# Optimization experiments

Measured on AMD Instinct MI355X. Metric: run time of the kernel, lower is better.

Reference implementation:

```python
import jax, jax.numpy as jnp
import numpy as np

TREE_DEPTH = 6
TEMPERATURE = 1.0


def setup_inputs() -> dict:
    key = jax.random.key(0)
    k1, k2, k3, k4, k5 = jax.random.split(key, 5)
    B, D = 8192, 512
    T = 64                      # n_trees
    N = 2 ** TREE_DEPTH - 1    # internal nodes = 63
    L = 2 ** TREE_DEPTH        # leaves = 64
    C = 100                    # classes
    return {
        "x": jax.random.normal(k1, (B, D), dtype=jnp.float32),
        "split_weights": jax.random.normal(k2, (T, N, D), dtype=jnp.float32),
        "split_bias": jax.random.normal(k3, (T, N), dtype=jnp.float32),
        "leaf_logits": jax.random.normal(k4, (T, L, C), dtype=jnp.float32),
        "tree_weights": jax.random.uniform(k5, (T,), dtype=jnp.float32),
    }


def reference(x, split_weights, split_bias, leaf_logits, tree_weights):
    # All node decisions for all trees in one batched GEMM: [B, T, N]
    dec = jax.nn.sigmoid(
        (jnp.einsum("bd,tnd->btn", x, split_weights) + split_bias) / TEMPERATURE
    )
    B = x.shape[0]
    T = split_weights.shape[0]
    L = leaf_logits.shape[1]  # 2 ** TREE_DEPTH
    leaf_ids = jnp.arange(L)
    # Cumulative product of routing probs along each leaf's root-to-leaf path.
    leaf_probs = jnp.ones((B, T, L), dtype=x.dtype)
    for d in range(TREE_DEPTH):
        # ancestor node (level order) of each leaf at this depth
        node_idx = (2 ** d - 1) + (leaf_ids >> (TREE_DEPTH - d))
        # 1 -> right child (prob = dec), 0 -> left child (prob = 1 - dec)
        bit = (leaf_ids >> (TREE_DEPTH - d - 1)) & 1
        dd = dec[:, :, node_idx]  # [B, T, L]
        leaf_probs = leaf_probs * jnp.where(bit.astype(bool), dd, 1.0 - dd)
    tree_out = jax.nn.softmax(leaf_logits, axis=-1)  # [T, L, C]
    # weighted sum over trees of (leaf_probs @ leaf class dists)
    return jnp.einsum("btl,tlc,t->bc", leaf_probs, tree_out, tree_weights)
```

## Files before the change

### kernel.cpp

```cpp
#include <hip/hip_runtime.h>

#define TREES 64
#define NN 63
#define LL 64
#define CC 100
#define CPAD 112
#define DD 512
#define BB 8192

typedef __attribute__((ext_vector_type(8))) _Float16 f16x8;
typedef __attribute__((ext_vector_type(4))) _Float16 f16x4;
typedef __attribute__((ext_vector_type(4))) float floatx4;

#define XH_WS   0
#define SWH_WS  8388608
#define W2T_WS  12582912

__device__ __forceinline__ void gl_lds16(const _Float16* g, char* lds) {
    __builtin_amdgcn_global_load_lds(
        (const __attribute__((address_space(1))) unsigned int*)g,
        (__attribute__((address_space(3))) unsigned int*)lds, 16, 0, 0);
}

__device__ __forceinline__ f16x8 cvt8(const float* s) {
    float4 a = *(const float4*)s, b = *(const float4*)(s + 4);
    f16x8 h;
    h[0]=(_Float16)a.x; h[1]=(_Float16)a.y; h[2]=(_Float16)a.z; h[3]=(_Float16)a.w;
    h[4]=(_Float16)b.x; h[5]=(_Float16)b.y; h[6]=(_Float16)b.z; h[7]=(_Float16)b.w;
    return h;
}

__device__ __forceinline__ float fsig(float x) {
    return __builtin_amdgcn_rcpf(1.f + __expf(-x));
}

__global__ __launch_bounds__(256) void prep_kernel(
    const float* __restrict__ x, const float* __restrict__ sw,
    const float* __restrict__ leaf_logits, const float* __restrict__ tree_w,
    _Float16* __restrict__ xh, _Float16* __restrict__ swh,
    _Float16* __restrict__ w2T, float* __restrict__ out)
{
    if (blockIdx.x < 3072) {
        int i = blockIdx.x * 256 + threadIdx.x;
        if (i < 524288) {
            int tile = i >> 10, cidx = i & 1023;
            int row = cidx >> 3, c = cidx & 7;
            int rb = tile >> 3, kt = tile & 7;
            int gk = kt * 64 + ((c ^ (row & 7)) << 3);
            *(f16x8*)(xh + (size_t)i * 8) = cvt8(x + (size_t)(rb * 128 + row) * DD + gk);
        } else {
            int j = i - 524288;
            if (j < 262144) {
                int tile = j >> 10, cidx = j & 1023;
                int col = cidx >> 3, c = cidx & 7;
                int cb = tile >> 3, kt = tile & 7;
                int tt = col >> 6, node = col & 63;
                f16x8 h = (f16x8)(_Float16)0.f;
                if (node < NN) {
                    int gk = kt * 64 + ((c ^ (col & 7)) << 3);
                    h = cvt8(sw + (size_t)((cb * 2 + tt) * NN + node) * DD + gk);
                }
                *(f16x8*)(swh + (size_t)j * 8) = h;
            }
        }
    } else if (blockIdx.x < 4096) {
        int row  = (blockIdx.x - 3072) * 4 + (threadIdx.x >> 6);
        int lane = threadIdx.x & 63;
        int t = row >> 6, l = row & 63;
        const float* src = leaf_logits + (size_t)row * CC;
        float v0 = (lane < CC)      ? src[lane]      : -1e30f;
        float v1 = (lane + 64 < CC) ? src[lane + 64] : -1e30f;
        float m = fmaxf(v0, v1);
#pragma unroll
        for (int off = 32; off > 0; off >>= 1)
            m = fmaxf(m, __shfl_down(m, off, 64));
        m = __shfl(m, 0, 64);
        float e0 = (lane < CC)      ? __expf(v0 - m) : 0.f;
        float e1 = (lane + 64 < CC) ? __expf(v1 - m) : 0.f;
        float s = e0 + e1;
#pragma unroll
        for (int off = 32; off > 0; off >>= 1)
            s += __shfl_down(s, off, 64);
        s = __shfl(s, 0, 64);
        float scale = tree_w[t] / s;
        _Float16* base = w2T + (size_t)t * CPAD * LL;
#define LSWZ(c) ((((l >> 3) ^ ((c) & 7)) << 3) | (l & 7))
        if (lane < CC)      base[(size_t)lane * LL + LSWZ(lane)]               = (_Float16)(e0 * scale);
        if (lane + 64 < CC) base[(size_t)(lane + 64) * LL + LSWZ(lane + 64)]   = (_Float16)(e1 * scale);
        if (lane < CPAD - CC) base[(size_t)(CC + lane) * LL + LSWZ(CC + lane)] = (_Float16)0.f;
#undef LSWZ
    } else {
        int i = (blockIdx.x - 4096) * 1024 + threadIdx.x * 4;
        *(float4*)(out + i) = make_float4(0.f, 0.f, 0.f, 0.f);
    }
}

#define A_SMEM 33280
__global__ __launch_bounds__(256, 2) void fused_kernel(
    const _Float16* __restrict__ xh,
    const _Float16* __restrict__ swh,
    const float* __restrict__ sb,
    const _Float16* __restrict__ w2T,
    float* __restrict__ out)
{
    __shared__ __align__(16) char smem[A_SMEM];
    _Float16* xs  = (_Float16*)smem;
    _Float16* wl  = (_Float16*)(smem + 16384);
    _Float16* dec = (_Float16*)smem;
    _Float16* lpl = (_Float16*)smem;

    const int tid  = threadIdx.x;
    const int lane = tid & 63;
    const int wid  = tid >> 6;
    const int wy   = wid >> 1;
    const int wx   = wid & 1;
    const int quad = lane >> 4;
    const int l15  = lane & 15;
    const int rb   = blockIdx.x;
    const int tc   = blockIdx.y;

    floatx4 oacc2[2][7];
#pragma unroll
    for (int mi = 0; mi < 2; ++mi)
#pragma unroll
        for (int ni = 0; ni < 7; ++ni) oacc2[mi][ni] = (floatx4)0.f;

    const _Float16* xtile = xh + (size_t)rb * 8 * 8192;

    for (int tg = 0; tg < 4; ++tg) {
        const int cb = tc * 4 + tg;
        const _Float16* wtile = swh + (size_t)cb * 8 * 8192;

        float bias_v[4];
        {
            int mytree = cb * 2 + wx;
#pragma unroll
            for (int ni = 0; ni < 4; ++ni) {
                int nd = 16 * ni + l15;
                bias_v[ni] = (nd < NN) ? sb[mytree * NN + nd] : 0.f;
            }
        }

        floatx4 acc[4][4];
#pragma unroll
        for (int i = 0; i < 4; ++i)
#pragma unroll
            for (int j = 0; j < 4; ++j) acc[i][j] = (floatx4)0.f;

        for (int kt = 0; kt < 8; ++kt) {
            __syncthreads();
#pragma unroll
            for (int j = 0; j < 4; ++j) {
                gl_lds16(xtile + kt * 8192 + j * 2048 + wid * 512 + lane * 8,
                         smem + j * 4096 + wid * 1024);
                gl_lds16(wtile + kt * 8192 + j * 2048 + wid * 512 + lane * 8,
                         smem + 16384 + j * 4096 + wid * 1024);
            }
            __syncthreads();
#pragma unroll
            for (int ks = 0; ks < 2; ++ks) {
                f16x8 af[4], bf[4];
#pragma unroll
                for (int mi = 0; mi < 4; ++mi) {
                    int r = 64 * wy + 16 * mi + l15;
                    af[mi] = *(const f16x8*)&xs[r * 64 + ((((ks << 2) | quad) ^ (r & 7)) << 3)];
                }
#pragma unroll
                for (int ni = 0; ni < 4; ++ni) {
                    int r = 64 * wx + 16 * ni + l15;
                    bf[ni] = *(const f16x8*)&wl[r * 64 + ((((ks << 2) | quad) ^ (r & 7)) << 3)];
                }
#pragma unroll
                for (int mi = 0; mi < 4; ++mi)
#pragma unroll
                    for (int ni = 0; ni < 4; ++ni)
                        acc[mi][ni] = __builtin_amdgcn_mfma_f32_16x16x32_f16(
                            af[mi], bf[ni], acc[mi][ni], 0, 0, 0);
            }
        }
        __syncthreads();

#pragma unroll
        for (int mi = 0; mi < 4; ++mi) {
            int r0 = 64 * wy + 16 * mi + 4 * quad;
#pragma unroll
            for (int ni = 0; ni < 4; ++ni) {
                int col = 64 * wx + 16 * ni + l15;
                f16x4 v;
#pragma unroll
                for (int r = 0; r < 4; ++r)
                    v[r] = (_Float16)(acc[mi][ni][r] + bias_v[ni]);
                *(f16x4*)&dec[col * 130 + r0] = v;
            }
        }
        __syncthreads();

        const int tt   = tid >> 7;
        const int lrow = tid & 127;
        const int tb   = tt * 64;
        f16x8 lpreg[8];
        {
#define SIG(n) fsig((float)dec[(tb + (n)) * 130 + lrow])
            float d0 = SIG(0);
#pragma unroll
            for (int h = 0; h < 2; ++h) {
                float p1 = h ? d0 : 1.f - d0;
                float d1 = SIG(1 + h);
#pragma unroll
                for (int b8 = 0; b8 < 4; ++b8) {
                    int i4 = b8 >> 1, i3 = b8 & 1;
                    float p2 = p1 * (i4 ? d1 : 1.f - d1);
                    float d2 = SIG(3 + 2 * h + i4);
                    float p3 = p2 * (i3 ? d2 : 1.f - d2);
                    float d3 = SIG(7 + 4 * h + b8);
                    f16x8 blk;
#pragma unroll
                    for (int i2 = 0; i2 < 2; ++i2) {
                        float p4 = p3 * (i2 ? d3 : 1.f - d3);
                        float d4 = SIG(15 + 8 * h + 2 * b8 + i2);
#pragma unroll
                        for (int i1 = 0; i1 < 2; ++i1) {
                            float p5 = p4 * (i1 ? d4 : 1.f - d4);
                            float d5 = SIG(31 + 16 * h + 4 * b8 + 2 * i2 + i1);
                            blk[i2 * 4 + i1 * 2 + 0] = (_Float16)(p5 * (1.f - d5));
                            blk[i2 * 4 + i1 * 2 + 1] = (_Float16)(p5 * d5);
                        }
                    }
                    lpreg[h * 4 + b8] = blk;
                }
            }
#undef SIG
        }
        __syncthreads();

#pragma unroll
        for (int q = 0; q < 8; ++q)
            *(f16x8*)&lpl[tt * 8192 + lrow * 64 + ((q ^ (lrow & 7)) << 3)] = lpreg[q];
        __syncthreads();

        {
            const int tree0 = cb * 2;
            const int rbase = wid * 32;
#pragma unroll
            for (int t = 0; t < 2; ++t) {
                const _Float16* bp = w2T + (size_t)(tree0 + t) * (CPAD * LL) + (size_t)l15 * 64;
                const _Float16* lplt = lpl + t * 8192;
#pragma unroll
                for (int ks = 0; ks < 2; ++ks) {
                    const int sw = (((ks << 2) | quad) ^ (l15 & 7)) << 3;
                    f16x8 bbv[7], abv[2];
#pragma unroll
                    for (int ni = 0; ni < 7; ++ni)
                        bbv[ni] = *(const f16x8*)(bp + ni * 16 * 64 + sw);
#pragma unroll
                    for (int mi = 0; mi < 2; ++mi) {
                        int r = rbase + 16 * mi + l15;
                        abv[mi] = *(const f16x8*)&lplt[r * 64 + sw];
                    }
#pragma unroll
                    for (int mi = 0; mi < 2; ++mi)
#pragma unroll
                        for (int ni = 0; ni < 7; ++ni)
                            oacc2[mi][ni] = __builtin_amdgcn_mfma_f32_16x16x32_f16(
                                abv[mi], bbv[ni], oacc2[mi][ni], 0, 0, 0);
                }
            }
        }
    }

    {
        const int rbase2 = rb * 128 + wid * 32 + 4 * quad;
#pragma unroll
        for (int mi = 0; mi < 2; ++mi)
#pragma unroll
            for (int ni = 0; ni < 7; ++ni) {
                int col = 16 * ni + l15;
                if (col < CC) {
#pragma unroll
                    for (int r = 0; r < 4; ++r)
                        unsafeAtomicAdd(&out[(size_t)(rbase2 + 16 * mi + r) * CC + col],
                                        oacc2[mi][ni][r]);
                }
            }
    }
}

extern "C" void kernel_launch(void* const* d_in, const int* in_sizes, int n_in,
                              void* d_out, int out_size, void* d_ws, size_t ws_size,
                              hipStream_t stream) {
    const float* x  = (const float*)d_in[0];
    const float* sw = (const float*)d_in[1];
    const float* sb = (const float*)d_in[2];
    const float* ll = (const float*)d_in[3];
    const float* tw = (const float*)d_in[4];
    float* out = (float*)d_out;
    _Float16* xh  = (_Float16*)((char*)d_ws + XH_WS);
    _Float16* swh = (_Float16*)((char*)d_ws + SWH_WS);
    _Float16* w2T = (_Float16*)((char*)d_ws + W2T_WS);

    prep_kernel<<<dim3(4896), 256, 0, stream>>>(x, sw, ll, tw, xh, swh, w2T, out);
    fused_kernel<<<dim3(64, 8), 256, 0, stream>>>(xh, swh, sb, w2T, out);
}
```

Before: 177.8 us.

## Double fused kernel block to 512 threads with finer per-wave work split

The fused kernel now runs 8 waves per block instead of 4. Each wave computes half as many GEMM1 output columns, half of a tree's leaf-probability expansion, and 16 instead of 32 rows of the second GEMM. The aim is more waves in flight to hide latency with the same grid of 512 blocks, and less register pressure per thread. In exchange, each wave does less MFMA work per LDS fragment load, barriers span more waves, and launch_bounds(512,4) asks for tighter register limits.

```diff
diff --git a/kernel.cpp b/kernel.cpp
--- a/kernel.cpp
+++ b/kernel.cpp
@@ -96,7 +96,7 @@
 }
 
 #define A_SMEM 33280
-__global__ __launch_bounds__(256, 2) void fused_kernel(
+__global__ __launch_bounds__(512, 4) void fused_kernel(
     const _Float16* __restrict__ xh,
     const _Float16* __restrict__ swh,
     const float* __restrict__ sb,
@@ -112,18 +112,16 @@
     const int tid  = threadIdx.x;
     const int lane = tid & 63;
     const int wid  = tid >> 6;
-    const int wy   = wid >> 1;
-    const int wx   = wid & 1;
+    const int wy   = wid >> 2;
+    const int wx   = wid & 3;
     const int quad = lane >> 4;
     const int l15  = lane & 15;
     const int rb   = blockIdx.x;
     const int tc   = blockIdx.y;
 
-    floatx4 oacc2[2][7];
-#pragma unroll
-    for (int mi = 0; mi < 2; ++mi)
-#pragma unroll
-        for (int ni = 0; ni < 7; ++ni) oacc2[mi][ni] = (floatx4)0.f;
+    floatx4 oacc2[7];
+#pragma unroll
+    for (int ni = 0; ni < 7; ++ni) oacc2[ni] = (floatx4)0.f;
 
     const _Float16* xtile = xh + (size_t)rb * 8 * 8192;
 
@@ -131,49 +129,49 @@
         const int cb = tc * 4 + tg;
         const _Float16* wtile = swh + (size_t)cb * 8 * 8192;
 
-        float bias_v[4];
+        float bias_v[2];
         {
-            int mytree = cb * 2 + wx;
-#pragma unroll
-            for (int ni = 0; ni < 4; ++ni) {
-                int nd = 16 * ni + l15;
+            int mytree = cb * 2 + (wx >> 1);
+#pragma unroll
+            for (int ni = 0; ni < 2; ++ni) {
+                int nd = 32 * (wx & 1) + 16 * ni + l15;
                 bias_v[ni] = (nd < NN) ? sb[mytree * NN + nd] : 0.f;
             }
         }
 
-        floatx4 acc[4][4];
+        floatx4 acc[4][2];
 #pragma unroll
         for (int i = 0; i < 4; ++i)
 #pragma unroll
-            for (int j = 0; j < 4; ++j) acc[i][j] = (floatx4)0.f;
+            for (int j = 0; j < 2; ++j) acc[i][j] = (floatx4)0.f;
 
         for (int kt = 0; kt < 8; ++kt) {
             __syncthreads();
 #pragma unroll
-            for (int j = 0; j < 4; ++j) {
-                gl_lds16(xtile + kt * 8192 + j * 2048 + wid * 512 + lane * 8,
-                         smem + j * 4096 + wid * 1024);
-                gl_lds16(wtile + kt * 8192 + j * 2048 + wid * 512 + lane * 8,
-                         smem + 16384 + j * 4096 + wid * 1024);
+            for (int j = 0; j < 2; ++j) {
+                gl_lds16(xtile + kt * 8192 + j * 4096 + wid * 512 + lane * 8,
+                         smem + j * 8192 + wid * 1024);
+                gl_lds16(wtile + kt * 8192 + j * 4096 + wid * 512 + lane * 8,
+                         smem + 16384 + j * 8192 + wid * 1024);
             }
             __syncthreads();
 #pragma unroll
             for (int ks = 0; ks < 2; ++ks) {
-                f16x8 af[4], bf[4];
+                f16x8 af[4], bf[2];
 #pragma unroll
                 for (int mi = 0; mi < 4; ++mi) {
                     int r = 64 * wy + 16 * mi + l15;
                     af[mi] = *(const f16x8*)&xs[r * 64 + ((((ks << 2) | quad) ^ (r & 7)) << 3)];
                 }
 #pragma unroll
-                for (int ni = 0; ni < 4; ++ni) {
-                    int r = 64 * wx + 16 * ni + l15;
+                for (int ni = 0; ni < 2; ++ni) {
+                    int r = 32 * wx + 16 * ni + l15;
                     bf[ni] = *(const f16x8*)&wl[r * 64 + ((((ks << 2) | quad) ^ (r & 7)) << 3)];
                 }
 #pragma unroll
                 for (int mi = 0; mi < 4; ++mi)
 #pragma unroll
-                    for (int ni = 0; ni < 4; ++ni)
+                    for (int ni = 0; ni < 2; ++ni)
                         acc[mi][ni] = __builtin_amdgcn_mfma_f32_16x16x32_f16(
                             af[mi], bf[ni], acc[mi][ni], 0, 0, 0);
             }
@@ -184,8 +182,8 @@
         for (int mi = 0; mi < 4; ++mi) {
             int r0 = 64 * wy + 16 * mi + 4 * quad;
 #pragma unroll
-            for (int ni = 0; ni < 4; ++ni) {
-                int col = 64 * wx + 16 * ni + l15;
+            for (int ni = 0; ni < 2; ++ni) {
+                int col = 32 * wx + 16 * ni + l15;
                 f16x4 v;
 #pragma unroll
                 for (int r = 0; r < 4; ++r)
@@ -195,52 +193,52 @@
         }
         __syncthreads();
 
-        const int tt   = tid >> 7;
+        const int u    = tid >> 8;
+        const int tt   = (tid >> 7) & 1;
         const int lrow = tid & 127;
         const int tb   = tt * 64;
-        f16x8 lpreg[8];
+        f16x8 lpreg[4];
         {
 #define SIG(n) fsig((float)dec[(tb + (n)) * 130 + lrow])
             float d0 = SIG(0);
-#pragma unroll
-            for (int h = 0; h < 2; ++h) {
-                float p1 = h ? d0 : 1.f - d0;
-                float d1 = SIG(1 + h);
-#pragma unroll
-                for (int b8 = 0; b8 < 4; ++b8) {
-                    int i4 = b8 >> 1, i3 = b8 & 1;
-                    float p2 = p1 * (i4 ? d1 : 1.f - d1);
-                    float d2 = SIG(3 + 2 * h + i4);
-                    float p3 = p2 * (i3 ? d2 : 1.f - d2);
-                    float d3 = SIG(7 + 4 * h + b8);
-                    f16x8 blk;
-#pragma unroll
-                    for (int i2 = 0; i2 < 2; ++i2) {
-                        float p4 = p3 * (i2 ? d3 : 1.f - d3);
-                        float d4 = SIG(15 + 8 * h + 2 * b8 + i2);
-#pragma unroll
-                        for (int i1 = 0; i1 < 2; ++i1) {
-                            float p5 = p4 * (i1 ? d4 : 1.f - d4);
-                            float d5 = SIG(31 + 16 * h + 4 * b8 + 2 * i2 + i1);
-                            blk[i2 * 4 + i1 * 2 + 0] = (_Float16)(p5 * (1.f - d5));
-                            blk[i2 * 4 + i1 * 2 + 1] = (_Float16)(p5 * d5);
-                        }
+            float p1 = u ? d0 : 1.f - d0;
+            float d1 = SIG(1 + u);
+#pragma unroll
+            for (int b8 = 0; b8 < 4; ++b8) {
+                int i4 = b8 >> 1, i3 = b8 & 1;
+                float p2 = p1 * (i4 ? d1 : 1.f - d1);
+                float d2 = SIG(3 + 2 * u + i4);
+                float p3 = p2 * (i3 ? d2 : 1.f - d2);
+                float d3 = SIG(7 + 4 * u + b8);
+                f16x8 blk;
+#pragma unroll
+                for (int i2 = 0; i2 < 2; ++i2) {
+                    float p4 = p3 * (i2 ? d3 : 1.f - d3);
+                    float d4 = SIG(15 + 8 * u + 2 * b8 + i2);
+#pragma unroll
+                    for (int i1 = 0; i1 < 2; ++i1) {
+                        float p5 = p4 * (i1 ? d4 : 1.f - d4);
+                        float d5 = SIG(31 + 16 * u + 4 * b8 + 2 * i2 + i1);
+                        blk[i2 * 4 + i1 * 2 + 0] = (_Float16)(p5 * (1.f - d5));
+                        blk[i2 * 4 + i1 * 2 + 1] = (_Float16)(p5 * d5);
                     }
-                    lpreg[h * 4 + b8] = blk;
-                }
+                }
+                lpreg[b8] = blk;
             }
 #undef SIG
         }
         __syncthreads();
 
 #pragma unroll
-        for (int q = 0; q < 8; ++q)
-            *(f16x8*)&lpl[tt * 8192 + lrow * 64 + ((q ^ (lrow & 7)) << 3)] = lpreg[q];
+        for (int b8 = 0; b8 < 4; ++b8) {
+            int q = u * 4 + b8;
+            *(f16x8*)&lpl[tt * 8192 + lrow * 64 + ((q ^ (lrow & 7)) << 3)] = lpreg[b8];
+        }
         __syncthreads();
 
         {
             const int tree0 = cb * 2;
-            const int rbase = wid * 32;
+            const int rbase = wid * 16;
 #pragma unroll
             for (int t = 0; t < 2; ++t) {
                 const _Float16* bp = w2T + (size_t)(tree0 + t) * (CPAD * LL) + (size_t)l15 * 64;
@@ -248,40 +246,32 @@
 #pragma unroll
                 for (int ks = 0; ks < 2; ++ks) {
                     const int sw = (((ks << 2) | quad) ^ (l15 & 7)) << 3;
-                    f16x8 bbv[7], abv[2];
+                    f16x8 bbv[7], abv;
 #pragma unroll
                     for (int ni = 0; ni < 7; ++ni)
                         bbv[ni] = *(const f16x8*)(bp + ni * 16 * 64 + sw);
-#pragma unroll
-                    for (int mi = 0; mi < 2; ++mi) {
-                        int r = rbase + 16 * mi + l15;
-                        abv[mi] = *(const f16x8*)&lplt[r * 64 + sw];
-                    }
-#pragma unroll
-                    for (int mi = 0; mi < 2; ++mi)
-#pragma unroll
-                        for (int ni = 0; ni < 7; ++ni)
-                            oacc2[mi][ni] = __builtin_amdgcn_mfma_f32_16x16x32_f16(
-                                abv[mi], bbv[ni], oacc2[mi][ni], 0, 0, 0);
+                    abv = *(const f16x8*)&lplt[(rbase + l15) * 64 + sw];
+#pragma unroll
+                    for (int ni = 0; ni < 7; ++ni)
+                        oacc2[ni] = __builtin_amdgcn_mfma_f32_16x16x32_f16(
+                            abv, bbv[ni], oacc2[ni], 0, 0, 0);
                 }
             }
         }
     }
 
     {
-        const int rbase2 = rb * 128 + wid * 32 + 4 * quad;
-#pragma unroll
-        for (int mi = 0; mi < 2; ++mi)
-#pragma unroll
-            for (int ni = 0; ni < 7; ++ni) {
-                int col = 16 * ni + l15;
-                if (col < CC) {
-#pragma unroll
-                    for (int r = 0; r < 4; ++r)
-                        unsafeAtomicAdd(&out[(size_t)(rbase2 + 16 * mi + r) * CC + col],
-                                        oacc2[mi][ni][r]);
-                }
-            }
+        const int rbase2 = rb * 128 + wid * 16 + 4 * quad;
+#pragma unroll
+        for (int ni = 0; ni < 7; ++ni) {
+            int col = 16 * ni + l15;
+            if (col < CC) {
+#pragma unroll
+                for (int r = 0; r < 4; ++r)
+                    unsafeAtomicAdd(&out[(size_t)(rbase2 + r) * CC + col],
+                                    oacc2[ni][r]);
+            }
+        }
     }
 }
 
@@ -299,5 +289,5 @@
     _Float16* w2T = (_Float16*)((char*)d_ws + W2T_WS);
 
     prep_kernel<<<dim3(4896), 256, 0, stream>>>(x, sw, ll, tw, xh, swh, w2T, out);
-    fused_kernel<<<dim3(64, 8), 256, 0, stream>>>(xh, swh, sb, w2T, out);
-}
+    fused_kernel<<<dim3(64, 8), 512, 0, stream>>>(xh, swh, sb, w2T, out);
+}
```

Result: slower. 191.8 us (+7.9%).
